# Kernel tuning notes

Hardware: AMD Instinct MI355X
Metric: run time of the kernel (lower is better)

The kernel has to match this reference:

```python
import jax, jax.numpy as jnp
import numpy as np

N_NODES = 10000


def _sage_pool(h, src, dst, Wp, bp, Ws, Wn, b):
    # DGL SAGEConv 'pool': m = relu(fc_pool(h_src)); neigh = max over in-edges;
    # out = fc_self(h_dst) + fc_neigh(neigh) + bias. Zero-in-degree nodes get 0 neigh.
    m = jax.nn.relu(h @ Wp + bp)                      # [N, d_in] node-level transform
    neigh = jax.ops.segment_max(m[src], dst, num_segments=N_NODES)  # [N, d_in]
    neigh = jnp.where(jnp.isfinite(neigh), neigh, 0.0)  # empty segments filled -inf -> 0
    return h @ Ws + neigh @ Wn + b


def setup_inputs() -> dict:
    key = jax.random.key(0)
    ks = jax.random.split(key, 20)
    dims = [(960, 512), (512, 512), (512, 1)]
    inp = {
        "h": jax.random.normal(ks[0], (N_NODES, 960), dtype=jnp.float32),
        "src": jax.random.randint(ks[1], (160000,), 0, N_NODES),
        "dst": jax.random.randint(ks[2], (160000,), 0, N_NODES),
    }
    ki = 3
    for l, (di, do) in enumerate(dims):
        inp[f"Wp{l}"] = jax.random.normal(ks[ki + 0], (di, di), dtype=jnp.float32) * 0.02
        inp[f"bp{l}"] = jnp.zeros((di,), dtype=jnp.float32)
        inp[f"Ws{l}"] = jax.random.normal(ks[ki + 1], (di, do), dtype=jnp.float32) * 0.02
        inp[f"Wn{l}"] = jax.random.normal(ks[ki + 2], (di, do), dtype=jnp.float32) * 0.02
        inp[f"b{l}"] = jnp.zeros((do,), dtype=jnp.float32)
        ki += 3
    return inp


def reference(h, src, dst,
              Wp0, bp0, Ws0, Wn0, b0,
              Wp1, bp1, Ws1, Wn1, b1,
              Wp2, bp2, Ws2, Wn2, b2):
    # layer 0: 960 -> 512, relu (dropout = identity in eval)
    x = jax.nn.relu(_sage_pool(h, src, dst, Wp0, bp0, Ws0, Wn0, b0))
    # layer 1: 512 -> 512, relu
    x = jax.nn.relu(_sage_pool(x, src, dst, Wp1, bp1, Ws1, Wn1, b1))
    # layer 2: 512 -> 1, sigmoid, squeeze -> per-node prediction
    x = _sage_pool(x, src, dst, Wp2, bp2, Ws2, Wn2, b2)
    return jax.nn.sigmoid(x).squeeze(-1)  # [N]
```

## Files before the change

kernel.cpp:

```cpp
#include <hip/hip_runtime.h>
#include <stdint.h>

#define NN 10000
#define NE 160000
#define MPAD 10112
#define MTILES 79

typedef unsigned short u16;
typedef float f32x4 __attribute__((ext_vector_type(4)));
typedef short short8 __attribute__((ext_vector_type(8)));
typedef __bf16 bf16x8 __attribute__((ext_vector_type(8)));
typedef unsigned short u16x4 __attribute__((ext_vector_type(4)));
typedef unsigned short u16x8 __attribute__((ext_vector_type(8)));

__device__ __forceinline__ float bf2f(u16 u) {
  union { unsigned u; float f; } c; c.u = ((unsigned)u) << 16; return c.f;
}
__device__ __forceinline__ u16 f2bf(float f) {
  union { float f; unsigned u; } c; c.f = f;
  return (u16)((c.u + 0x7FFFu + ((c.u >> 16) & 1u)) >> 16);
}

__device__ __forceinline__ void gld_lds16(void* lds, const void* g) {
  __builtin_amdgcn_global_load_lds(
      (const unsigned int __attribute__((address_space(1)))*)g,
      (unsigned int __attribute__((address_space(3)))*)lds, 16, 0, 0);
}

__global__ __launch_bounds__(256) void deg_count(const int* __restrict__ dst, int* __restrict__ deg) {
  int e = blockIdx.x * 256 + threadIdx.x;
  if (e < NE) atomicAdd(&deg[dst[e]], 1);
}

__global__ __launch_bounds__(256) void scan_off(const int* __restrict__ deg,
                                                int* __restrict__ roff, int* __restrict__ cur) {
  __shared__ int part[256];
  const int t = threadIdx.x;
  const int CH = 40;
  int s = 0;
  for (int i = 0; i < CH; ++i) { int idx = t * CH + i; if (idx < NN) s += deg[idx]; }
  part[t] = s; __syncthreads();
  for (int off = 1; off < 256; off <<= 1) {
    int v = (t >= off) ? part[t - off] : 0;
    __syncthreads(); part[t] += v; __syncthreads();
  }
  int run = (t == 0) ? 0 : part[t - 1];
  for (int i = 0; i < CH; ++i) {
    int idx = t * CH + i;
    if (idx < NN) { roff[idx] = run; cur[idx] = run; run += deg[idx]; }
  }
  if (t == 255) roff[NN] = NE;
}

__global__ __launch_bounds__(256) void fill_csr(const int* __restrict__ src, const int* __restrict__ dst,
                                                int* __restrict__ cur, int* __restrict__ esrc) {
  int e = blockIdx.x * 256 + threadIdx.x;
  if (e < NE) {
    int p = atomicAdd(&cur[dst[e]], 1);
    esrc[p] = src[e];
  }
}

__global__ __launch_bounds__(256) void convert_h(const float* __restrict__ h, u16* __restrict__ hbf) {
  const size_t i = (size_t)(blockIdx.x * 256 + threadIdx.x) * 4;
  if (i >= (size_t)MPAD * 960) return;
  u16x4 o;
  if (i < (size_t)NN * 960) {
    float4 v = *(const float4*)(h + i);
    o[0] = f2bf(v.x); o[1] = f2bf(v.y); o[2] = f2bf(v.z); o[3] = f2bf(v.w);
  } else {
    o[0] = 0; o[1] = 0; o[2] = 0; o[3] = 0;
  }
  *(u16x4*)(hbf + i) = o;
}

struct WDesc { const float* in; u16* out; int R, C, Cpad, ldo, koff; };
struct WPack { WDesc d[7]; };

__global__ __launch_bounds__(256) void transpose_all(WPack p) {
  const WDesc w = p.d[blockIdx.z];
  const int cb = blockIdx.x * 32, rb = blockIdx.y * 32;
  if (cb >= w.Cpad || rb >= w.R) return;
  __shared__ float tile[32][33];
  const int tx = threadIdx.x & 31, ty = threadIdx.x >> 5;
  for (int i = ty; i < 32; i += 8) {
    int r = rb + i, c = cb + tx;
    tile[i][tx] = (r < w.R && c < w.C) ? w.in[(size_t)r * w.C + c] : 0.f;
  }
  __syncthreads();
  for (int i = ty; i < 32; i += 8) {
    int c = cb + i, r = rb + tx;
    if (c < w.Cpad && r < w.R) w.out[(size_t)c * w.ldo + w.koff + r] = f2bf(tile[tx][i]);
  }
}

template<int TM, int TN, int MINB>
__global__ __launch_bounds__(256, MINB) void gemm3(
    const u16* __restrict__ A0, int lda0,
    const u16* __restrict__ A1, int lda1, int ksplit,
    const u16* __restrict__ B,
    const float* __restrict__ bias, int nbias,
    u16* __restrict__ Cb, int ldcb,
    int K, int act, int tiles_n) {
  constexpr int TR = TM + TN;
  constexpr int NC = TR / 64;
  constexpr int WCOLS = (TM == 128) ? 2 : 4;
  constexpr int WN = TN / WCOLS;
  constexpr int NJ = WN / 16;
  constexpr int MT = MPAD / TM;
  __shared__ __align__(16) u16 S0[TR * 32];
  __shared__ __align__(16) u16 S1[TR * 32];
  __shared__ __align__(16) u16 S2[TR * 32];
  const int tid = threadIdx.x;
  const int wave = tid >> 6, lane = tid & 63;

  const int nwg = tiles_n * MT;
  const int orig = blockIdx.x + blockIdx.y * tiles_n;
  const int q = nwg >> 3, r8 = nwg & 7;
  const int xcd = orig & 7, idx = orig >> 3;
  const int wg = (xcd < r8 ? xcd * (q + 1) : r8 * (q + 1) + (xcd - r8) * q) + idx;
  const int tm = (wg / tiles_n) * TM;
  const int tn = (wg % tiles_n) * TN;

  const int wr = (wave / WCOLS) * 64;
  const int wc = (wave % WCOLS) * WN;
  const int fr = lane & 15, fq = lane >> 4;
  const int sr16 = lane >> 2;
  const int sslot = lane & 3;
  f32x4 acc[4][NJ] = {};

  auto stage = [&](u16* Sw, int kk) {
#pragma unroll
    for (int c = 0; c < NC; ++c) {
      const int row = c * 64 + wave * 16 + sr16;
      const int gs = (sslot ^ ((row >> 1) & 3)) * 8;
      const void* g;
      if (c < TM / 64) {
        g = (kk < ksplit)
            ? (const void*)&A0[(size_t)(tm + row) * lda0 + kk + gs]
            : (const void*)&A1[(size_t)(tm + row) * lda1 + (kk - ksplit) + gs];
      } else {
        g = (const void*)&B[(size_t)(tn + row - TM) * (size_t)K + kk + gs];
      }
      gld_lds16(&Sw[(c * 64 + wave * 16) * 32], g);
    }
  };

  const int nsteps = K >> 5;
  stage(S0, 0);
  stage(S1, 32);
  for (int base = 0; base < nsteps; base += 3) {
#pragma unroll
    for (int ph = 0; ph < 3; ++ph) {
      const int t = base + ph;
      if (t >= nsteps) break;
      const u16* Sr = (ph == 0) ? S0 : (ph == 1) ? S1 : S2;
      u16*       Sw = (ph == 0) ? S2 : (ph == 1) ? S0 : S1;
      if (t + 1 < nsteps) {
        asm volatile("s_waitcnt vmcnt(%0)" :: "i"(NC) : "memory");
      } else {
        asm volatile("s_waitcnt vmcnt(0)" ::: "memory");
      }
      __builtin_amdgcn_s_barrier();
      __builtin_amdgcn_sched_barrier(0);
      short8 af[4], bfr[NJ];
#pragma unroll
      for (int i = 0; i < 4; ++i) {
        const int r = wr + i * 16 + fr;
        af[i] = *(const short8*)&Sr[r * 32 + ((fq ^ ((r >> 1) & 3)) << 3)];
      }
#pragma unroll
      for (int j = 0; j < NJ; ++j) {
        const int r = TM + wc + j * 16 + fr;
        bfr[j] = *(const short8*)&Sr[r * 32 + ((fq ^ ((r >> 1) & 3)) << 3)];
      }
      __builtin_amdgcn_sched_barrier(0);
      if (t + 2 < nsteps) stage(Sw, (t + 2) << 5);
      __builtin_amdgcn_s_setprio(1);
#pragma unroll
      for (int i = 0; i < 4; ++i)
#pragma unroll
        for (int j = 0; j < NJ; ++j)
          acc[i][j] = __builtin_amdgcn_mfma_f32_16x16x32_bf16(
              __builtin_bit_cast(bf16x8, af[i]), __builtin_bit_cast(bf16x8, bfr[j]),
              acc[i][j], 0, 0, 0);
      __builtin_amdgcn_s_setprio(0);
      __builtin_amdgcn_sched_barrier(0);
    }
  }

  const int cr = fq * 4, cc = fr;
#pragma unroll
  for (int i = 0; i < 4; ++i)
#pragma unroll
    for (int j = 0; j < NJ; ++j) {
      const int col = tn + wc + j * 16 + cc;
      const float bv = (col < nbias) ? bias[col] : 0.f;
#pragma unroll
      for (int r = 0; r < 4; ++r) {
        const int row = tm + wr + i * 16 + cr + r;
        float v = acc[i][j][r] + bv;
        if (act) v = fmaxf(v, 0.f);
        Cb[(size_t)row * ldcb + col] = f2bf(v);
      }
    }
}

template<int CW>
__global__ __launch_bounds__(256) void aggregate_xcd(
    const u16* __restrict__ m, int ldm, const int* __restrict__ roff,
    const int* __restrict__ esrc, u16* __restrict__ neigh, int ldn) {
  constexpr int TPN = CW / 8;
  constexpr int NPB = 256 / TPN;
  const int chunk = blockIdx.x & 7;
  const int node = (blockIdx.x >> 3) * NPB + threadIdx.x / TPN;
  if (node >= NN) return;
  const int fi = chunk * CW + (threadIdx.x % TPN) * 8;
  const int beg = roff[node], end = roff[node + 1];
  u16x8 a;
#pragma unroll
  for (int i = 0; i < 8; ++i) a[i] = 0;
  for (int e = beg; e < end; ++e) {
    const u16* row = m + (size_t)esrc[e] * ldm;
    u16x8 v = *(const u16x8*)(row + fi);
#pragma unroll
    for (int i = 0; i < 8; ++i) a[i] = (v[i] > a[i]) ? v[i] : a[i];
  }
  *(u16x8*)(neigh + (size_t)node * ldn + fi) = a;
}

__global__ __launch_bounds__(256) void final_out(
    const u16* __restrict__ x, const u16* __restrict__ neigh,
    const float* __restrict__ ws, const float* __restrict__ wn,
    const float* __restrict__ b, float* __restrict__ out) {
  const int wave = threadIdx.x >> 6, lane = threadIdx.x & 63;
  const int n = blockIdx.x * 4 + wave;
  if (n >= NN) return;
  const int f = lane * 8;
  const u16* xr = x + (size_t)n * 512 + f;
  const u16* nr = neigh + (size_t)n * 512 + f;
  float s = 0.f;
#pragma unroll
  for (int i = 0; i < 8; ++i)
    s += bf2f(xr[i]) * ws[f + i] + bf2f(nr[i]) * wn[f + i];
#pragma unroll
  for (int o = 32; o > 0; o >>= 1) s += __shfl_xor(s, o);
  if (lane == 0) out[n] = 1.f / (1.f + expf(-(s + b[0])));
}

extern "C" void kernel_launch(void* const* d_in, const int* in_sizes, int n_in,
                              void* d_out, int out_size, void* d_ws, size_t ws_size,
                              hipStream_t stream) {
  const float* h   = (const float*)d_in[0];
  const int*   src = (const int*)d_in[1];
  const int*   dst = (const int*)d_in[2];
  const float* Wp0 = (const float*)d_in[3];
  const float* bp0 = (const float*)d_in[4];
  const float* Ws0 = (const float*)d_in[5];
  const float* Wn0 = (const float*)d_in[6];
  const float* b0  = (const float*)d_in[7];
  const float* Wp1 = (const float*)d_in[8];
  const float* bp1 = (const float*)d_in[9];
  const float* Ws1 = (const float*)d_in[10];
  const float* Wn1 = (const float*)d_in[11];
  const float* b1  = (const float*)d_in[12];
  const float* Wp2 = (const float*)d_in[13];
  const float* bp2 = (const float*)d_in[14];
  const float* Ws2 = (const float*)d_in[15];
  const float* Wn2 = (const float*)d_in[16];
  const float* b2  = (const float*)d_in[17];
  float* out = (float*)d_out;

  char* ws = (char*)d_ws;
  size_t off = 0;
  auto alloc = [&](size_t n) { char* p = ws + off; off = (off + n + 255) & ~(size_t)255; return p; };
  u16* hbf   = (u16*)alloc((size_t)MPAD * 960 * 2);
  u16* x1    = (u16*)alloc((size_t)MPAD * 512 * 2);
  u16* x2    = (u16*)alloc((size_t)MPAD * 512 * 2);
  u16* mbuf  = (u16*)alloc((size_t)MPAD * 1024 * 2);
  u16* nbuf  = (u16*)alloc((size_t)MPAD * 1024 * 2);
  u16* WpT0  = (u16*)alloc((size_t)1024 * 960 * 2);
  u16* Bcat0 = (u16*)alloc((size_t)512 * 1920 * 2);
  u16* WpT1  = (u16*)alloc((size_t)512 * 512 * 2);
  u16* Bcat1 = (u16*)alloc((size_t)512 * 1024 * 2);
  u16* WpT2  = (u16*)alloc((size_t)512 * 512 * 2);
  int* deg   = (int*)alloc(NN * 4);
  int* roff  = (int*)alloc((NN + 1) * 4);
  int* curp  = (int*)alloc(NN * 4);
  int* esrc  = (int*)alloc(NE * 4);

  hipMemsetAsync(deg, 0, NN * 4, stream);
  deg_count<<<NE / 256, 256, 0, stream>>>(dst, deg);
  scan_off<<<1, 256, 0, stream>>>(deg, roff, curp);
  fill_csr<<<NE / 256, 256, 0, stream>>>(src, dst, curp, esrc);
  convert_h<<<(MPAD * 960 / 4) / 256, 256, 0, stream>>>(h, hbf);

  WPack wp;
  wp.d[0] = {Wp0, WpT0,  960, 960, 1024,  960,   0};
  wp.d[1] = {Ws0, Bcat0, 960, 512,  512, 1920,   0};
  wp.d[2] = {Wn0, Bcat0, 960, 512,  512, 1920, 960};
  wp.d[3] = {Wp1, WpT1,  512, 512,  512,  512,   0};
  wp.d[4] = {Ws1, Bcat1, 512, 512,  512, 1024,   0};
  wp.d[5] = {Wn1, Bcat1, 512, 512,  512, 1024, 512};
  wp.d[6] = {Wp2, WpT2,  512, 512,  512,  512,   0};
  transpose_all<<<dim3(32, 30, 7), 256, 0, stream>>>(wp);

  gemm3<128, 128, 3><<<dim3(8, 79), 256, 0, stream>>>(
      hbf, 960, hbf, 960, 960, WpT0, bp0, 960, mbuf, 1024, 960, 1, 8);
  aggregate_xcd<128><<<5000, 256, 0, stream>>>(mbuf, 1024, roff, esrc, nbuf, 1024);
  gemm3<128, 128, 3><<<dim3(4, 79), 256, 0, stream>>>(
      hbf, 960, nbuf, 1024, 960, Bcat0, b0, 512, x1, 512, 1920, 1, 4);

  gemm3<128, 128, 3><<<dim3(4, 79), 256, 0, stream>>>(
      x1, 512, x1, 512, 512, WpT1, bp1, 512, mbuf, 512, 512, 1, 4);
  aggregate_xcd<64><<<2504, 256, 0, stream>>>(mbuf, 512, roff, esrc, nbuf, 512);
  gemm3<128, 128, 3><<<dim3(4, 79), 256, 0, stream>>>(
      x1, 512, nbuf, 512, 512, Bcat1, b1, 512, x2, 512, 1024, 1, 4);

  gemm3<128, 128, 3><<<dim3(4, 79), 256, 0, stream>>>(
      x2, 512, x2, 512, 512, WpT2, bp2, 512, mbuf, 512, 512, 1, 4);
  aggregate_xcd<64><<<2504, 256, 0, stream>>>(mbuf, 512, roff, esrc, nbuf, 512);
  final_out<<<2500, 256, 0, stream>>>(x2, nbuf, Ws2, Wn2, b2, out);
}
```

Measured before the change: 266.5 us.

## Switch GEMM to 64-wide K steps with double buffering and 8-way swizzle

The bf16 MFMA GEMM now stages 64 K-elements per step into two LDS buffers instead of 32 K-elements into three. The LDS XOR swizzle is widened from 4 to 8 slots, and launch bounds drop from 3 to 2 blocks per CU to fit the larger LDS footprint. The aim is to halve the number of barrier/wait phases per tile and double the MFMA work per phase. In exchange it adds a second barrier before the buffer is overwritten, which shortens the load/compute overlap, and it lowers occupancy.

Result: faster. 260.5 us (-2.2%).

```diff
diff --git a/kernel.cpp b/kernel.cpp
--- a/kernel.cpp
+++ b/kernel.cpp
@@ -103,14 +103,13 @@
     u16* __restrict__ Cb, int ldcb,
     int K, int act, int tiles_n) {
   constexpr int TR = TM + TN;
-  constexpr int NC = TR / 64;
+  constexpr int NC = TR / 32;
   constexpr int WCOLS = (TM == 128) ? 2 : 4;
   constexpr int WN = TN / WCOLS;
   constexpr int NJ = WN / 16;
   constexpr int MT = MPAD / TM;
-  __shared__ __align__(16) u16 S0[TR * 32];
-  __shared__ __align__(16) u16 S1[TR * 32];
-  __shared__ __align__(16) u16 S2[TR * 32];
+  __shared__ __align__(16) u16 S0[TR * 64];
+  __shared__ __align__(16) u16 S1[TR * 64];
   const int tid = threadIdx.x;
   const int wave = tid >> 6, lane = tid & 63;
 
@@ -125,37 +124,36 @@
   const int wr = (wave / WCOLS) * 64;
   const int wc = (wave % WCOLS) * WN;
   const int fr = lane & 15, fq = lane >> 4;
-  const int sr16 = lane >> 2;
-  const int sslot = lane & 3;
+  const int sr8 = lane >> 3;
+  const int sslot = lane & 7;
   f32x4 acc[4][NJ] = {};
 
   auto stage = [&](u16* Sw, int kk) {
 #pragma unroll
     for (int c = 0; c < NC; ++c) {
-      const int row = c * 64 + wave * 16 + sr16;
-      const int gs = (sslot ^ ((row >> 1) & 3)) * 8;
+      const int row = c * 32 + wave * 8 + sr8;
+      const int gs = (sslot ^ (row & 7)) * 8;
       const void* g;
-      if (c < TM / 64) {
+      if (c < NC * TM / TR) {
         g = (kk < ksplit)
             ? (const void*)&A0[(size_t)(tm + row) * lda0 + kk + gs]
             : (const void*)&A1[(size_t)(tm + row) * lda1 + (kk - ksplit) + gs];
       } else {
         g = (const void*)&B[(size_t)(tn + row - TM) * (size_t)K + kk + gs];
       }
-      gld_lds16(&Sw[(c * 64 + wave * 16) * 32], g);
+      gld_lds16(&Sw[(c * 32 + wave * 8) * 64], g);
     }
   };
 
-  const int nsteps = K >> 5;
+  const int nsteps = K >> 6;
   stage(S0, 0);
-  stage(S1, 32);
-  for (int base = 0; base < nsteps; base += 3) {
-#pragma unroll
-    for (int ph = 0; ph < 3; ++ph) {
+  stage(S1, 64);
+  for (int base = 0; base < nsteps; base += 2) {
+#pragma unroll
+    for (int ph = 0; ph < 2; ++ph) {
       const int t = base + ph;
       if (t >= nsteps) break;
-      const u16* Sr = (ph == 0) ? S0 : (ph == 1) ? S1 : S2;
-      u16*       Sw = (ph == 0) ? S2 : (ph == 1) ? S0 : S1;
+      u16* Sr = (ph == 0) ? S0 : S1;
       if (t + 1 < nsteps) {
         asm volatile("s_waitcnt vmcnt(%0)" :: "i"(NC) : "memory");
       } else {
@@ -163,27 +161,35 @@
       }
       __builtin_amdgcn_s_barrier();
       __builtin_amdgcn_sched_barrier(0);
-      short8 af[4], bfr[NJ];
+      short8 af[4][2], bfr[2][NJ];
 #pragma unroll
       for (int i = 0; i < 4; ++i) {
         const int r = wr + i * 16 + fr;
-        af[i] = *(const short8*)&Sr[r * 32 + ((fq ^ ((r >> 1) & 3)) << 3)];
+#pragma unroll
+        for (int kc = 0; kc < 2; ++kc)
+          af[i][kc] = *(const short8*)&Sr[r * 64 + ((((kc << 2) | fq) ^ (r & 7)) << 3)];
       }
 #pragma unroll
       for (int j = 0; j < NJ; ++j) {
         const int r = TM + wc + j * 16 + fr;
-        bfr[j] = *(const short8*)&Sr[r * 32 + ((fq ^ ((r >> 1) & 3)) << 3)];
-      }
+#pragma unroll
+        for (int kc = 0; kc < 2; ++kc)
+          bfr[kc][j] = *(const short8*)&Sr[r * 64 + ((((kc << 2) | fq) ^ (r & 7)) << 3)];
+      }
+      asm volatile("s_waitcnt lgkmcnt(0)" ::: "memory");
       __builtin_amdgcn_sched_barrier(0);
-      if (t + 2 < nsteps) stage(Sw, (t + 2) << 5);
+      __builtin_amdgcn_s_barrier();
+      if (t + 2 < nsteps) stage(Sr, (t + 2) << 6);
       __builtin_amdgcn_s_setprio(1);
 #pragma unroll
-      for (int i = 0; i < 4; ++i)
-#pragma unroll
-        for (int j = 0; j < NJ; ++j)
-          acc[i][j] = __builtin_amdgcn_mfma_f32_16x16x32_bf16(
-              __builtin_bit_cast(bf16x8, af[i]), __builtin_bit_cast(bf16x8, bfr[j]),
-              acc[i][j], 0, 0, 0);
+      for (int kc = 0; kc < 2; ++kc)
+#pragma unroll
+        for (int i = 0; i < 4; ++i)
+#pragma unroll
+          for (int j = 0; j < NJ; ++j)
+            acc[i][j] = __builtin_amdgcn_mfma_f32_16x16x32_bf16(
+                __builtin_bit_cast(bf16x8, af[i][kc]), __builtin_bit_cast(bf16x8, bfr[kc][j]),
+                acc[i][j], 0, 0, 0);
       __builtin_amdgcn_s_setprio(0);
       __builtin_amdgcn_sched_barrier(0);
     }
@@ -305,19 +311,19 @@
   wp.d[6] = {Wp2, WpT2,  512, 512,  512,  512,   0};
   transpose_all<<<dim3(32, 30, 7), 256, 0, stream>>>(wp);
 
-  gemm3<128, 128, 3><<<dim3(8, 79), 256, 0, stream>>>(
+  gemm3<128, 128, 2><<<dim3(8, 79), 256, 0, stream>>>(
       hbf, 960, hbf, 960, 960, WpT0, bp0, 960, mbuf, 1024, 960, 1, 8);
   aggregate_xcd<128><<<5000, 256, 0, stream>>>(mbuf, 1024, roff, esrc, nbuf, 1024);
-  gemm3<128, 128, 3><<<dim3(4, 79), 256, 0, stream>>>(
+  gemm3<128, 128, 2><<<dim3(4, 79), 256, 0, stream>>>(
       hbf, 960, nbuf, 1024, 960, Bcat0, b0, 512, x1, 512, 1920, 1, 4);
 
-  gemm3<128, 128, 3><<<dim3(4, 79), 256, 0, stream>>>(
+  gemm3<128, 128, 2><<<dim3(4, 79), 256, 0, stream>>>(
       x1, 512, x1, 512, 512, WpT1, bp1, 512, mbuf, 512, 512, 1, 4);
   aggregate_xcd<64><<<2504, 256, 0, stream>>>(mbuf, 512, roff, esrc, nbuf, 512);
-  gemm3<128, 128, 3><<<dim3(4, 79), 256, 0, stream>>>(
+  gemm3<128, 128, 2><<<dim3(4, 79), 256, 0, stream>>>(
       x1, 512, nbuf, 512, 512, Bcat1, b1, 512, x2, 512, 1024, 1, 4);
 
-  gemm3<128, 128, 3><<<dim3(4, 79), 256, 0, stream>>>(
+  gemm3<128, 128, 2><<<dim3(4, 79), 256, 0, stream>>>(
       x2, 512, x2, 512, 512, WpT2, bp2, 512, mbuf, 512, 512, 1, 4);
   aggregate_xcd<64><<<2504, 256, 0, stream>>>(mbuf, 512, roff, esrc, nbuf, 512);
   final_out<<<2500, 256, 0, stream>>>(x2, nbuf, Ws2, Wn2, b2, out);
```
